# Kernel tuning notes

Measured on AMD Instinct MI355X. Metric: run time of the kernel, lower is better.

The kernel has to match this reference:

```python
import jax, jax.numpy as jnp
import numpy as np

WS = (8, 8)  # window_size
NUM_HEADS = 6


def _relative_position_index(ws):
    ch, cw = np.arange(ws[0]), np.arange(ws[1])
    coords = np.stack(np.meshgrid(ch, cw, indexing='ij'))  # [2, Wh, Ww]
    cf = coords.reshape(2, -1)  # [2, N]
    rel = cf[:, :, None] - cf[:, None, :]  # [2, N, N]
    rel = rel.transpose(1, 2, 0).astype(np.int64)
    rel[:, :, 0] += ws[0] - 1
    rel[:, :, 1] += ws[1] - 1
    rel[:, :, 0] *= 2 * ws[1] - 1
    return rel.sum(-1)  # [N, N]

_RPI = jnp.asarray(_relative_position_index(WS))  # [64, 64] int


def setup_inputs() -> dict:
    key = jax.random.key(0)
    ks = jax.random.split(key, 6)
    B_, N, C = 4096, WS[0] * WS[1], 192
    return {
        'x': jax.random.normal(ks[0], (B_, N, C), jnp.float32),
        'qkv_w': jax.random.normal(ks[1], (3 * C, C), jnp.float32) * 0.02,
        'qkv_b': jax.random.normal(ks[2], (3 * C,), jnp.float32) * 0.02,
        'proj_w': jax.random.normal(ks[3], (C, C), jnp.float32) * 0.02,
        'proj_b': jax.random.normal(ks[4], (C,), jnp.float32) * 0.02,
        'rpb_table': jax.random.normal(ks[5], ((2 * WS[0] - 1) * (2 * WS[1] - 1), NUM_HEADS), jnp.float32) * 0.02,
    }


def reference(x, qkv_w, qkv_b, proj_w, proj_b, rpb_table):
    B_, N, C = x.shape
    H = NUM_HEADS
    D = C // H
    scale = D ** (-0.5)
    # qkv: torch Linear -> x @ W^T + b
    qkv = (x @ qkv_w.T + qkv_b).reshape(B_, N, 3, H, D)
    qkv = jnp.transpose(qkv, (2, 0, 3, 1, 4))  # [3, B_, H, N, D]
    q, k, v = qkv[0] * scale, qkv[1], qkv[2]
    attn = jnp.einsum('bhnd,bhmd->bhnm', q, k)  # [B_, H, N, N]
    bias = rpb_table[_RPI]  # [N, N, H]
    attn = attn + jnp.transpose(bias, (2, 0, 1))[None]  # broadcast over B_
    attn = jax.nn.softmax(attn, axis=-1)
    out = jnp.einsum('bhnm,bhmd->bnhd', attn, v).reshape(B_, N, C)
    return out @ proj_w.T + proj_b
```

## Files before the change

kernel.cpp:

```cpp
#include <hip/hip_runtime.h>
#include <hip/hip_bf16.h>

typedef short bf16x8 __attribute__((ext_vector_type(8)));
typedef float f32x4 __attribute__((ext_vector_type(4)));
typedef unsigned int u32;
typedef unsigned int u32x2 __attribute__((ext_vector_type(2)));

#define MFMA16 __builtin_amdgcn_mfma_f32_16x16x32_bf16
#define SCALE 0.17677669529663687f


__device__ __forceinline__ unsigned short f2b(float x) {
  u32 u = __float_as_uint(x);
  u = (u + 0x7FFFu + ((u >> 16) & 1u)) >> 16;
  return (unsigned short)u;
}
__device__ __forceinline__ u32 pk2(float a, float b) {
  __hip_bfloat162 h = __float22bfloat162_rn(float2{a, b});
  return *(u32*)&h;
}

__device__ __forceinline__ bf16x8 xpose(f32x4 a0, f32x4 a1) {
  u32 s0 = pk2(a0[0], a0[1]);
  u32 s1 = pk2(a0[2], a0[3]);
  u32 s2 = pk2(a1[0], a1[1]);
  u32 s3 = pk2(a1[2], a1[3]);
  u32x2 r0 = __builtin_amdgcn_permlane16_swap(s0, s2, false, false);
  u32x2 r1 = __builtin_amdgcn_permlane16_swap(s1, s3, false, false);
  union {
    u32 w[4];
    bf16x8 v;
  } u;
  u.w[0] = r0[0];
  u.w[1] = r1[0];
  u.w[2] = r0[1];
  u.w[3] = r1[1];
  return u.v;
}

__global__ void prep_kernel(const float* __restrict__ qkv_w, const float* __restrict__ qkv_b,
                            const float* __restrict__ proj_w, const float* __restrict__ rpb,
                            unsigned short* __restrict__ wqkv, unsigned short* __restrict__ wproj,
                            float* __restrict__ biasar, float* __restrict__ bq) {
  int i0 = blockIdx.x * blockDim.x + threadIdx.x;
  int stride = gridDim.x * blockDim.x;
  for (int i = i0; i < 576 * 192; i += stride) {
    float v = qkv_w[i];
    if (i < 192 * 192) v *= SCALE;
    wqkv[i] = f2b(v);
  }
  for (int i = i0; i < 192 * 192; i += stride) wproj[i] = f2b(proj_w[i]);
  for (int i = i0; i < 576; i += stride) {
    float v = qkv_b[i];
    if (i < 192) v *= SCALE;
    bq[i] = v;
  }
  for (int i = i0; i < 6 * 16 * 64 * 4; i += stride) {
    int r = i & 3;
    int lane = (i >> 2) & 63;
    int fid = (i >> 8) & 15;
    int h = i >> 12;
    int mt = fid >> 2, nt = fid & 3;
    int m = mt * 16 + (lane >> 4) * 4 + r;
    int n = nt * 16 + (lane & 15);
    int idx = ((n >> 3) - (m >> 3) + 7) * 15 + ((n & 7) - (m & 7) + 7);
    biasar[i] = rpb[idx * 6 + h];
  }
}

__global__ void __launch_bounds__(384, 3) win_attn(
    const float* __restrict__ x, const unsigned short* __restrict__ wqkv,
    const unsigned short* __restrict__ wproj, const float* __restrict__ biasar,
    const float* __restrict__ bq, const float* __restrict__ proj_b, float* __restrict__ out) {
  __shared__ __align__(16) char smem[24576];
  const int b = blockIdx.x;
  const int tid = threadIdx.x;
  const int w = tid >> 6;
  const int lane = tid & 63;
  const int g = lane >> 4;
  const int c = lane & 15;
  char* xs = smem;

  {
    const float* xb = x + (size_t)b * 12288;
#pragma unroll
    for (int it = 0; it < 8; ++it) {
      int idx = tid + it * 384;
      int tok = idx / 48, c4 = idx % 48;
      float4 v = *(const float4*)(xb + tok * 192 + c4 * 4);
      *(uint2*)(xs + tok * 384 + (((c4 >> 1) ^ (tok & 7)) << 4) + (c4 & 1) * 8) =
          make_uint2(pk2(v.x, v.y), pk2(v.z, v.w));
    }
  }
  __syncthreads();

#define XFRAG(tt, kt) \
  (*(const bf16x8*)(xs + ((tt) * 16 + c) * 384 + ((((kt) * 4 + g) ^ (c & 7)) << 4)))

  bf16x8 qb[4];
  {
    f32x4 acc[2][4];
#pragma unroll
    for (int dt = 0; dt < 2; ++dt)
#pragma unroll
      for (int tt = 0; tt < 4; ++tt) acc[dt][tt] = (f32x4)0.0f;
#pragma unroll
    for (int kt = 0; kt < 6; ++kt) {
      bf16x8 wf[2];
#pragma unroll
      for (int dt = 0; dt < 2; ++dt)
        wf[dt] = *(const bf16x8*)(wqkv + (size_t)(w * 32 + dt * 16 + c) * 192 + kt * 32 + 8 * g);
#pragma unroll
      for (int tt = 0; tt < 4; ++tt) {
        bf16x8 xf = XFRAG(tt, kt);
#pragma unroll
        for (int dt = 0; dt < 2; ++dt) acc[dt][tt] = MFMA16(wf[dt], xf, acc[dt][tt], 0, 0, 0);
      }
    }
#pragma unroll
    for (int dt = 0; dt < 2; ++dt)
#pragma unroll
      for (int r = 0; r < 4; ++r) {
        float bv = bq[w * 32 + dt * 16 + 4 * g + r];
#pragma unroll
        for (int tt = 0; tt < 4; ++tt) acc[dt][tt][r] += bv;
      }
#pragma unroll
    for (int nt = 0; nt < 4; ++nt) qb[nt] = xpose(acc[0][nt], acc[1][nt]);
  }

  bf16x8 ka[4];
  {
    f32x4 acc[2][4];
#pragma unroll
    for (int dt = 0; dt < 2; ++dt)
#pragma unroll
      for (int tt = 0; tt < 4; ++tt) acc[dt][tt] = (f32x4)0.0f;
#pragma unroll
    for (int kt = 0; kt < 6; ++kt) {
      bf16x8 wf[2];
#pragma unroll
      for (int dt = 0; dt < 2; ++dt)
        wf[dt] =
            *(const bf16x8*)(wqkv + (size_t)(192 + w * 32 + dt * 16 + c) * 192 + kt * 32 + 8 * g);
#pragma unroll
      for (int tt = 0; tt < 4; ++tt) {
        bf16x8 xf = XFRAG(tt, kt);
#pragma unroll
        for (int dt = 0; dt < 2; ++dt) acc[dt][tt] = MFMA16(wf[dt], xf, acc[dt][tt], 0, 0, 0);
      }
    }
#pragma unroll
    for (int dt = 0; dt < 2; ++dt)
#pragma unroll
      for (int r = 0; r < 4; ++r) {
        float bv = bq[192 + w * 32 + dt * 16 + 4 * g + r];
#pragma unroll
        for (int tt = 0; tt < 4; ++tt) acc[dt][tt][r] += bv;
      }
#pragma unroll
    for (int mt = 0; mt < 4; ++mt) ka[mt] = xpose(acc[0][mt], acc[1][mt]);
  }

  bf16x8 pbf[2][4];
  float linv[4];
  const f32x4* bias4 = (const f32x4*)biasar;
#pragma unroll
  for (int h = 0; h < 2; ++h) {
    f32x4 s[4][2];
#pragma unroll
    for (int mt = 0; mt < 4; ++mt)
#pragma unroll
      for (int n2 = 0; n2 < 2; ++n2) {
        int nt = h * 2 + n2;
        f32x4 t = MFMA16(ka[mt], qb[nt], (f32x4)0.0f, 0, 0, 0);
        s[mt][n2] = t + bias4[(w * 16 + mt * 4 + nt) * 64 + lane];
      }
#pragma unroll
    for (int n2 = 0; n2 < 2; ++n2) {
      int nt = h * 2 + n2;
      float mx = -1e30f;
#pragma unroll
      for (int mt = 0; mt < 4; ++mt)
#pragma unroll
        for (int r = 0; r < 4; ++r) mx = fmaxf(mx, s[mt][n2][r]);
      mx = fmaxf(mx, __shfl_xor(mx, 16));
      mx = fmaxf(mx, __shfl_xor(mx, 32));
      float sum = 0.0f;
#pragma unroll
      for (int mt = 0; mt < 4; ++mt)
#pragma unroll
        for (int r = 0; r < 4; ++r) {
          float e = __expf(s[mt][n2][r] - mx);
          s[mt][n2][r] = e;
          sum += e;
        }
      sum += __shfl_xor(sum, 16);
      sum += __shfl_xor(sum, 32);
      linv[nt] = 1.0f / sum;
    }
#pragma unroll
    for (int n2 = 0; n2 < 2; ++n2) {
      pbf[0][h * 2 + n2] = xpose(s[0][n2], s[1][n2]);
      pbf[1][h * 2 + n2] = xpose(s[2][n2], s[3][n2]);
    }
  }

  bf16x8 va[2][2];
  {
    f32x4 acc[4][2];
#pragma unroll
    for (int mt = 0; mt < 4; ++mt)
#pragma unroll
      for (int dt = 0; dt < 2; ++dt) acc[mt][dt] = (f32x4)0.0f;
#pragma unroll
    for (int kt = 0; kt < 6; ++kt) {
      bf16x8 wf[2];
#pragma unroll
      for (int dt = 0; dt < 2; ++dt)
        wf[dt] =
            *(const bf16x8*)(wqkv + (size_t)(384 + w * 32 + dt * 16 + c) * 192 + kt * 32 + 8 * g);
#pragma unroll
      for (int tt = 0; tt < 4; ++tt) {
        bf16x8 xf = XFRAG(tt, kt);
#pragma unroll
        for (int dt = 0; dt < 2; ++dt) acc[tt][dt] = MFMA16(xf, wf[dt], acc[tt][dt], 0, 0, 0);
      }
    }
#pragma unroll
    for (int dt = 0; dt < 2; ++dt) {
      float bv = bq[384 + w * 32 + dt * 16 + c];
#pragma unroll
      for (int mt = 0; mt < 4; ++mt)
#pragma unroll
        for (int r = 0; r < 4; ++r) acc[mt][dt][r] += bv;
    }
#pragma unroll
    for (int dt = 0; dt < 2; ++dt)
#pragma unroll
      for (int kh = 0; kh < 2; ++kh) va[dt][kh] = xpose(acc[2 * kh][dt], acc[2 * kh + 1][dt]);
  }

  f32x4 o[2][4];
#pragma unroll
  for (int dt = 0; dt < 2; ++dt)
#pragma unroll
    for (int nt = 0; nt < 4; ++nt) o[dt][nt] = (f32x4)0.0f;
#pragma unroll
  for (int mh = 0; mh < 2; ++mh)
#pragma unroll
    for (int nt = 0; nt < 4; ++nt)
#pragma unroll
      for (int dt = 0; dt < 2; ++dt) o[dt][nt] = MFMA16(va[dt][mh], pbf[mh][nt], o[dt][nt], 0, 0, 0);
#pragma unroll
  for (int dt = 0; dt < 2; ++dt)
#pragma unroll
    for (int nt = 0; nt < 4; ++nt)
#pragma unroll
      for (int r = 0; r < 4; ++r) o[dt][nt][r] *= linv[nt];

  __syncthreads();
#pragma unroll
  for (int dt = 0; dt < 2; ++dt)
#pragma unroll
    for (int nt = 0; nt < 4; ++nt)
      *(uint2*)(xs + (nt * 16 + c) * 384 + (((w * 4 + dt * 2 + (g >> 1)) ^ (c & 7)) << 4) +
                (g & 1) * 8) = make_uint2(pk2(o[dt][nt][0], o[dt][nt][1]),
                                          pk2(o[dt][nt][2], o[dt][nt][3]));
  __syncthreads();

  f32x4 accP[4][2];
#pragma unroll
  for (int mt = 0; mt < 4; ++mt)
#pragma unroll
    for (int ft = 0; ft < 2; ++ft) accP[mt][ft] = (f32x4)0.0f;
#pragma unroll
  for (int kt = 0; kt < 6; ++kt) {
    bf16x8 wp[2];
#pragma unroll
    for (int ft = 0; ft < 2; ++ft)
      wp[ft] = *(const bf16x8*)(wproj + (size_t)(w * 32 + ft * 16 + c) * 192 + kt * 32 + 8 * g);
#pragma unroll
    for (int mt = 0; mt < 4; ++mt) {
      bf16x8 of = *(const bf16x8*)(xs + (mt * 16 + c) * 384 + (((kt * 4 + g) ^ (c & 7)) << 4));
#pragma unroll
      for (int ft = 0; ft < 2; ++ft) accP[mt][ft] = MFMA16(of, wp[ft], accP[mt][ft], 0, 0, 0);
    }
  }
  float pb0 = proj_b[w * 32 + c];
  float pb1 = proj_b[w * 32 + 16 + c];
  float* outb = out + (size_t)b * 12288;
#pragma unroll
  for (int mt = 0; mt < 4; ++mt)
#pragma unroll
    for (int ft = 0; ft < 2; ++ft) {
      float pbv = ft ? pb1 : pb0;
#pragma unroll
      for (int r = 0; r < 4; ++r)
        outb[(mt * 16 + 4 * g + r) * 192 + w * 32 + ft * 16 + c] = accP[mt][ft][r] + pbv;
    }
}

extern "C" void kernel_launch(void* const* d_in, const int* in_sizes, int n_in,
                              void* d_out, int out_size, void* d_ws, size_t ws_size,
                              hipStream_t stream) {
  const float* x = (const float*)d_in[0];
  const float* qkv_w = (const float*)d_in[1];
  const float* qkv_b = (const float*)d_in[2];
  const float* proj_w = (const float*)d_in[3];
  const float* proj_b = (const float*)d_in[4];
  const float* rpb = (const float*)d_in[5];
  char* ws = (char*)d_ws;
  unsigned short* wqkv = (unsigned short*)ws;
  unsigned short* wproj = (unsigned short*)(ws + 221184);
  float* biasar = (float*)(ws + 294912);
  float* bqv = (float*)(ws + 393216);

  prep_kernel<<<432, 256, 0, stream>>>(qkv_w, qkv_b, proj_w, rpb, wqkv, wproj, biasar, bqv);
  win_attn<<<4096, 384, 0, stream>>>(x, wqkv, wproj, biasar, bqv, proj_b, (float*)d_out);
}
```

Baseline: 323.2 us.

## Split window attention into per-head-group kernel and separate projection kernel

Replaces the fused per-window kernel with two kernels. The first runs two blocks per window, each covering three heads, and writes the bf16 attention output to a workspace buffer. A separate projection kernel reads that buffer back, reshuffles it into LDS and applies the output projection. The aim is smaller blocks and more parallelism, at the cost of loading x twice per window and an extra round trip of about 100 MB of intermediate data through global memory. The split path runs only when the workspace is large enough, otherwise the old fused kernel is used.

```diff
diff --git a/kernel.cpp b/kernel.cpp
--- a/kernel.cpp
+++ b/kernel.cpp
@@ -9,6 +9,8 @@
 #define MFMA16 __builtin_amdgcn_mfma_f32_16x16x32_bf16
 #define SCALE 0.17677669529663687f
 
+#define OS_OFF 395520
+#define WS_NEED (395520 + 100663296)
 
 __device__ __forceinline__ unsigned short f2b(float x) {
   u32 u = __float_as_uint(x);
@@ -18,6 +20,9 @@
 __device__ __forceinline__ u32 pk2(float a, float b) {
   __hip_bfloat162 h = __float22bfloat162_rn(float2{a, b});
   return *(u32*)&h;
+}
+__device__ __forceinline__ uint2 pk4(f32x4 v) {
+  return make_uint2(pk2(v[0], v[1]), pk2(v[2], v[3]));
 }
 
 __device__ __forceinline__ bf16x8 xpose(f32x4 a0, f32x4 a1) {
@@ -68,6 +73,262 @@
   }
 }
 
+__global__ void __launch_bounds__(192, 4) win_attn3(
+    const float* __restrict__ x, const unsigned short* __restrict__ wqkv,
+    const float* __restrict__ biasar, const float* __restrict__ bq,
+    unsigned short* __restrict__ osout) {
+  __shared__ __align__(16) char smem[24576];
+  const int bid = blockIdx.x;
+  const int b = bid >> 1;
+  const int hg = bid & 1;
+  const int tid = threadIdx.x;
+  const int w = tid >> 6;
+  const int head = hg * 3 + w;
+  const int lane = tid & 63;
+  const int g = lane >> 4;
+  const int c = lane & 15;
+  char* xs = smem;
+
+  {
+    const float* xb = x + (size_t)b * 12288;
+#pragma unroll
+    for (int it = 0; it < 16; ++it) {
+      int idx = tid + it * 192;
+      int tok = idx / 48, c4 = idx % 48;
+      float4 v = *(const float4*)(xb + tok * 192 + c4 * 4);
+      *(uint2*)(xs + tok * 384 + (((c4 >> 1) ^ (tok & 7)) << 4) + (c4 & 1) * 8) =
+          make_uint2(pk2(v.x, v.y), pk2(v.z, v.w));
+    }
+  }
+  __syncthreads();
+
+#define XFRAG(tt, kt) \
+  (*(const bf16x8*)(xs + ((tt) * 16 + c) * 384 + ((((kt) * 4 + g) ^ (c & 7)) << 4)))
+
+  bf16x8 qb[4];
+  {
+    f32x4 acc[2][4];
+#pragma unroll
+    for (int dt = 0; dt < 2; ++dt)
+#pragma unroll
+      for (int tt = 0; tt < 4; ++tt) acc[dt][tt] = (f32x4)0.0f;
+#pragma unroll
+    for (int kt = 0; kt < 6; ++kt) {
+      bf16x8 wf[2];
+#pragma unroll
+      for (int dt = 0; dt < 2; ++dt)
+        wf[dt] = *(const bf16x8*)(wqkv + (size_t)(head * 32 + dt * 16 + c) * 192 + kt * 32 + 8 * g);
+#pragma unroll
+      for (int tt = 0; tt < 4; ++tt) {
+        bf16x8 xf = XFRAG(tt, kt);
+#pragma unroll
+        for (int dt = 0; dt < 2; ++dt) acc[dt][tt] = MFMA16(wf[dt], xf, acc[dt][tt], 0, 0, 0);
+      }
+    }
+#pragma unroll
+    for (int dt = 0; dt < 2; ++dt)
+#pragma unroll
+      for (int r = 0; r < 4; ++r) {
+        float bv = bq[head * 32 + dt * 16 + 4 * g + r];
+#pragma unroll
+        for (int tt = 0; tt < 4; ++tt) acc[dt][tt][r] += bv;
+      }
+#pragma unroll
+    for (int nt = 0; nt < 4; ++nt) qb[nt] = xpose(acc[0][nt], acc[1][nt]);
+  }
+
+  bf16x8 ka[4];
+  {
+    f32x4 acc[2][4];
+#pragma unroll
+    for (int dt = 0; dt < 2; ++dt)
+#pragma unroll
+      for (int tt = 0; tt < 4; ++tt) acc[dt][tt] = (f32x4)0.0f;
+#pragma unroll
+    for (int kt = 0; kt < 6; ++kt) {
+      bf16x8 wf[2];
+#pragma unroll
+      for (int dt = 0; dt < 2; ++dt)
+        wf[dt] =
+            *(const bf16x8*)(wqkv + (size_t)(192 + head * 32 + dt * 16 + c) * 192 + kt * 32 + 8 * g);
+#pragma unroll
+      for (int tt = 0; tt < 4; ++tt) {
+        bf16x8 xf = XFRAG(tt, kt);
+#pragma unroll
+        for (int dt = 0; dt < 2; ++dt) acc[dt][tt] = MFMA16(wf[dt], xf, acc[dt][tt], 0, 0, 0);
+      }
+    }
+#pragma unroll
+    for (int dt = 0; dt < 2; ++dt)
+#pragma unroll
+      for (int r = 0; r < 4; ++r) {
+        float bv = bq[192 + head * 32 + dt * 16 + 4 * g + r];
+#pragma unroll
+        for (int tt = 0; tt < 4; ++tt) acc[dt][tt][r] += bv;
+      }
+#pragma unroll
+    for (int mt = 0; mt < 4; ++mt) ka[mt] = xpose(acc[0][mt], acc[1][mt]);
+  }
+
+  bf16x8 pbf[2][4];
+  float linv[4];
+  const f32x4* bias4 = (const f32x4*)biasar;
+#pragma unroll
+  for (int h = 0; h < 2; ++h) {
+    f32x4 s[4][2];
+#pragma unroll
+    for (int mt = 0; mt < 4; ++mt)
+#pragma unroll
+      for (int n2 = 0; n2 < 2; ++n2) {
+        int nt = h * 2 + n2;
+        f32x4 t = MFMA16(ka[mt], qb[nt], (f32x4)0.0f, 0, 0, 0);
+        s[mt][n2] = t + bias4[(head * 16 + mt * 4 + nt) * 64 + lane];
+      }
+#pragma unroll
+    for (int n2 = 0; n2 < 2; ++n2) {
+      int nt = h * 2 + n2;
+      float mx = -1e30f;
+#pragma unroll
+      for (int mt = 0; mt < 4; ++mt)
+#pragma unroll
+        for (int r = 0; r < 4; ++r) mx = fmaxf(mx, s[mt][n2][r]);
+      mx = fmaxf(mx, __shfl_xor(mx, 16));
+      mx = fmaxf(mx, __shfl_xor(mx, 32));
+      float sum = 0.0f;
+#pragma unroll
+      for (int mt = 0; mt < 4; ++mt)
+#pragma unroll
+        for (int r = 0; r < 4; ++r) {
+          float e = __expf(s[mt][n2][r] - mx);
+          s[mt][n2][r] = e;
+          sum += e;
+        }
+      sum += __shfl_xor(sum, 16);
+      sum += __shfl_xor(sum, 32);
+      linv[nt] = 1.0f / sum;
+    }
+#pragma unroll
+    for (int n2 = 0; n2 < 2; ++n2) {
+      pbf[0][h * 2 + n2] = xpose(s[0][n2], s[1][n2]);
+      pbf[1][h * 2 + n2] = xpose(s[2][n2], s[3][n2]);
+    }
+  }
+
+  bf16x8 va[2][2];
+  {
+    f32x4 acc[4][2];
+#pragma unroll
+    for (int mt = 0; mt < 4; ++mt)
+#pragma unroll
+      for (int dt = 0; dt < 2; ++dt) acc[mt][dt] = (f32x4)0.0f;
+#pragma unroll
+    for (int kt = 0; kt < 6; ++kt) {
+      bf16x8 wf[2];
+#pragma unroll
+      for (int dt = 0; dt < 2; ++dt)
+        wf[dt] =
+            *(const bf16x8*)(wqkv + (size_t)(384 + head * 32 + dt * 16 + c) * 192 + kt * 32 + 8 * g);
+#pragma unroll
+      for (int tt = 0; tt < 4; ++tt) {
+        bf16x8 xf = XFRAG(tt, kt);
+#pragma unroll
+        for (int dt = 0; dt < 2; ++dt) acc[tt][dt] = MFMA16(xf, wf[dt], acc[tt][dt], 0, 0, 0);
+      }
+    }
+#pragma unroll
+    for (int dt = 0; dt < 2; ++dt) {
+      float bv = bq[384 + head * 32 + dt * 16 + c];
+#pragma unroll
+      for (int mt = 0; mt < 4; ++mt)
+#pragma unroll
+        for (int r = 0; r < 4; ++r) acc[mt][dt][r] += bv;
+    }
+#pragma unroll
+    for (int dt = 0; dt < 2; ++dt)
+#pragma unroll
+      for (int kh = 0; kh < 2; ++kh) va[dt][kh] = xpose(acc[2 * kh][dt], acc[2 * kh + 1][dt]);
+  }
+
+  f32x4 o[2][4];
+#pragma unroll
+  for (int dt = 0; dt < 2; ++dt)
+#pragma unroll
+    for (int nt = 0; nt < 4; ++nt) o[dt][nt] = (f32x4)0.0f;
+#pragma unroll
+  for (int mh = 0; mh < 2; ++mh)
+#pragma unroll
+    for (int nt = 0; nt < 4; ++nt)
+#pragma unroll
+      for (int dt = 0; dt < 2; ++dt) o[dt][nt] = MFMA16(va[dt][mh], pbf[mh][nt], o[dt][nt], 0, 0, 0);
+
+  uint2* dst = (uint2*)osout + ((size_t)(b * 6 + head) * 8) * 64 + lane;
+#pragma unroll
+  for (int dt = 0; dt < 2; ++dt)
+#pragma unroll
+    for (int nt = 0; nt < 4; ++nt) {
+#pragma unroll
+      for (int r = 0; r < 4; ++r) o[dt][nt][r] *= linv[nt];
+      dst[(dt * 4 + nt) * 64] = pk4(o[dt][nt]);
+    }
+}
+
+__global__ void __launch_bounds__(256, 4) proj_kernel(
+    const unsigned short* __restrict__ osin, const unsigned short* __restrict__ wproj,
+    const float* __restrict__ proj_b, float* __restrict__ out) {
+  __shared__ __align__(16) char smem[24576];
+  const int b = blockIdx.x;
+  const int tid = threadIdx.x;
+  const int w = tid >> 6;
+  const int lane = tid & 63;
+  const int g = lane >> 4;
+  const int c = lane & 15;
+
+  {
+    const uint2* src = (const uint2*)osin + (size_t)b * 3072;
+#pragma unroll
+    for (int it = 0; it < 12; ++it) {
+      int i = tid + it * 256;
+      int ls = i & 63;
+      int frag = (i >> 6) & 7;
+      int head = i >> 9;
+      int tok = (frag & 3) * 16 + (ls & 15);
+      int d0 = head * 32 + (frag >> 2) * 16 + 4 * (ls >> 4);
+      uint2 v = src[i];
+      *(uint2*)(smem + tok * 384 + ((((d0 >> 3)) ^ (tok & 7)) << 4) + (d0 & 7) * 2) = v;
+    }
+  }
+  __syncthreads();
+
+  f32x4 acc[4][3];
+#pragma unroll
+  for (int mt = 0; mt < 4; ++mt)
+#pragma unroll
+    for (int ft = 0; ft < 3; ++ft) acc[mt][ft] = (f32x4)0.0f;
+#pragma unroll
+  for (int kt = 0; kt < 6; ++kt) {
+    bf16x8 wf[3];
+#pragma unroll
+    for (int ft = 0; ft < 3; ++ft)
+      wf[ft] = *(const bf16x8*)(wproj + (size_t)(w * 48 + ft * 16 + c) * 192 + kt * 32 + 8 * g);
+#pragma unroll
+    for (int mt = 0; mt < 4; ++mt) {
+      bf16x8 of = *(const bf16x8*)(smem + (mt * 16 + c) * 384 + (((kt * 4 + g) ^ (c & 7)) << 4));
+#pragma unroll
+      for (int ft = 0; ft < 3; ++ft) acc[mt][ft] = MFMA16(of, wf[ft], acc[mt][ft], 0, 0, 0);
+    }
+  }
+  float* outb = out + (size_t)b * 12288;
+#pragma unroll
+  for (int ft = 0; ft < 3; ++ft) {
+    float pbv = proj_b[w * 48 + ft * 16 + c];
+#pragma unroll
+    for (int mt = 0; mt < 4; ++mt)
+#pragma unroll
+      for (int r = 0; r < 4; ++r)
+        outb[(mt * 16 + 4 * g + r) * 192 + w * 48 + ft * 16 + c] = acc[mt][ft][r] + pbv;
+  }
+}
+
 __global__ void __launch_bounds__(384, 3) win_attn(
     const float* __restrict__ x, const unsigned short* __restrict__ wqkv,
     const unsigned short* __restrict__ wproj, const float* __restrict__ biasar,
@@ -94,9 +355,6 @@
   }
   __syncthreads();
 
-#define XFRAG(tt, kt) \
-  (*(const bf16x8*)(xs + ((tt) * 16 + c) * 384 + ((((kt) * 4 + g) ^ (c & 7)) << 4)))
-
   bf16x8 qb[4];
   {
     f32x4 acc[2][4];
@@ -265,8 +523,8 @@
 #pragma unroll
     for (int nt = 0; nt < 4; ++nt)
       *(uint2*)(xs + (nt * 16 + c) * 384 + (((w * 4 + dt * 2 + (g >> 1)) ^ (c & 7)) << 4) +
-                (g & 1) * 8) = make_uint2(pk2(o[dt][nt][0], o[dt][nt][1]),
-                                          pk2(o[dt][nt][2], o[dt][nt][3]));
+                (g & 1) * 8) =
+          make_uint2(pk2(o[dt][nt][0], o[dt][nt][1]), pk2(o[dt][nt][2], o[dt][nt][3]));
   __syncthreads();
 
   f32x4 accP[4][2];
@@ -317,5 +575,12 @@
   float* bqv = (float*)(ws + 393216);
 
   prep_kernel<<<432, 256, 0, stream>>>(qkv_w, qkv_b, proj_w, rpb, wqkv, wproj, biasar, bqv);
-  win_attn<<<4096, 384, 0, stream>>>(x, wqkv, wproj, biasar, bqv, proj_b, (float*)d_out);
-}
+
+  if (ws_size >= (size_t)WS_NEED) {
+    unsigned short* osbuf = (unsigned short*)(ws + OS_OFF);
+    win_attn3<<<8192, 192, 0, stream>>>(x, wqkv, biasar, bqv, osbuf);
+    proj_kernel<<<4096, 256, 0, stream>>>(osbuf, wproj, proj_b, (float*)d_out);
+  } else {
+    win_attn<<<4096, 384, 0, stream>>>(x, wqkv, wproj, biasar, bqv, proj_b, (float*)d_out);
+  }
+}
```

Result: slower. 573.5 us (+77.4%).
